# Kernel optimization log

Hardware: AMD Instinct MI355X
Metric: run time of the kernel (lower is better)

Reference implementation:

```python
import jax, jax.numpy as jnp
import numpy as np

N = 16384
K = 16

def _w(k, shape):
    return jax.random.normal(k, shape, jnp.float32) * 0.05

def setup_inputs() -> dict:
    key = jax.random.key(0)
    ks = jax.random.split(key, 20)
    return {
        "img_feat": jax.random.normal(ks[0], (1, 32, N), jnp.float32),
        "cloud": jax.random.uniform(ks[1], (1, N, 3), jnp.float32),
        "conv1_w": _w(ks[2], (64, 32)),   "conv1_b": _w(ks[3], (64,)),
        "conv2_w": _w(ks[4], (128, 64)),  "conv2_b": _w(ks[5], (128,)),
        "psconv1_w": _w(ks[6], (256, 128)), "psconv1_b": _w(ks[7], (256,)),
        "psconv2_w": _w(ks[8], (128, 256)), "psconv2_b": _w(ks[9], (128,)),
        "pconv1_w": _w(ks[10], (64, 3)),  "pconv1_b": _w(ks[11], (64,)),
        "pconv2_w": _w(ks[12], (128, 64)),"pconv2_b": _w(ks[13], (128,)),
        "final_w": _w(ks[14], (32, 416)), "final_b": _w(ks[15], (32,)),
        "topk": K,
    }

def reference(img_feat, cloud, conv1_w, conv1_b, conv2_w, conv2_b,
              psconv1_w, psconv1_b, psconv2_w, psconv2_b,
              pconv1_w, pconv1_b, pconv2_w, pconv2_b,
              final_w, final_b, topk):
    lrelu = lambda x: jax.nn.leaky_relu(x, 0.01)
    pts = cloud[0]            # [N,3]  (module assumes bs=1)
    imf = img_feat[0].T       # [N,32]
    # point MLP: pconv1 -> lrelu -> pconv2 (Conv1d kernel=1 == per-point linear)
    cf = lrelu(pts @ pconv1_w.T + pconv1_b) @ pconv2_w.T + pconv2_b  # [N,128]
    # KNN: k smallest euclidean distances (self included)
    sq = jnp.sum(pts * pts, axis=-1)                 # [N]
    d2 = sq[:, None] + sq[None, :] - 2.0 * (pts @ pts.T)  # [N,N]
    _, idx = jax.lax.top_k(-d2, topk)                # [N,K]
    nb_pts = pts[idx]                                # [N,K,3]
    dist = jnp.sqrt(jnp.maximum(jnp.sum((pts[:, None, :] - nb_pts) ** 2, -1), 1e-12))
    wgt = jax.nn.softmax(-dist, axis=1)              # [N,K]
    nb_img = imf[idx]                                # [N,K,32]
    nb_cf = cf[idx]                                  # [N,K,128]
    sf = lrelu(nb_img @ conv1_w.T + conv1_b) @ conv2_w.T + conv2_b         # [N,K,128]
    sfp = lrelu(nb_cf @ psconv1_w.T + psconv1_b) @ psconv2_w.T + psconv2_b # [N,K,128]
    sf = jnp.max(sf * wgt[:, :, None], axis=1)       # weighted max-pool -> [N,128]
    sfp = jnp.max(sfp * wgt[:, :, None], axis=1)     # [N,128]
    final = jnp.concatenate([sfp, imf, sf, cf], axis=1)  # [N,416]
    out = lrelu(final) @ final_w.T + final_b         # [N,32]
    return out.T[None]                               # [1,32,N]
```

## Files before the change

kernel.cpp:

```cpp
#include <hip/hip_runtime.h>
#include <math.h>

#define N 16384
#define KNN 16
#define G 16
#define NCELL 4096

typedef __attribute__((ext_vector_type(8))) short bf16x8;
typedef __attribute__((ext_vector_type(4))) float f32x4;
typedef unsigned short ushort_t;
typedef unsigned long long u64;

__device__ __forceinline__ float lrelu(float a) { return a > 0.f ? a : 0.01f * a; }

__device__ __forceinline__ ushort_t f2bf(float f) {
  unsigned u = __float_as_uint(f);
  u += 0x7FFF + ((u >> 16) & 1);
  return (ushort_t)(u >> 16);
}
__device__ __forceinline__ float bf2f(ushort_t h) {
  return __uint_as_float((unsigned)h << 16);
}
__device__ __forceinline__ int lanerank(u64 mask) {
  return __builtin_amdgcn_mbcnt_hi((unsigned)(mask >> 32),
         __builtin_amdgcn_mbcnt_lo((unsigned)mask, 0));
}
__device__ __forceinline__ int cellof(float x) {
  int c = (int)(x * (float)G);
  return c < 0 ? 0 : (c > G - 1 ? G - 1 : c);
}

#define PPB 64
__global__ __launch_bounds__(256) void prepw_kernel(
    const float* __restrict__ img, const float* __restrict__ cloud,
    const float* __restrict__ p1w, const float* __restrict__ p1b,
    const float* __restrict__ p2w, const float* __restrict__ p2b,
    const float* __restrict__ ps1w, const float* __restrict__ ps2w,
    const float* __restrict__ c1w, const float* __restrict__ c2w,
    const float* __restrict__ fw,
    float4* __restrict__ pts4, ushort_t* __restrict__ cfh,
    ushort_t* __restrict__ imfh,
    ushort_t* __restrict__ w1h, ushort_t* __restrict__ w2h,
    ushort_t* __restrict__ c1h, ushort_t* __restrict__ c2h,
    float* __restrict__ fwp2, int* __restrict__ count) {
  int t = threadIdx.x;
  if (blockIdx.x >= 256) {
    int e = (blockIdx.x - 256) * 256 + t;
    if (e < 32768) w1h[e] = f2bf(ps1w[e]);
    else if (e < 65536) w2h[e - 32768] = f2bf(ps2w[e - 32768]);
    else if (e < 67584) c1h[e - 65536] = f2bf(c1w[e - 65536]);
    else if (e < 75776) c2h[e - 67584] = f2bf(c2w[e - 67584]);
    else if (e < 89088) {
      int e2 = e - 75776;
      int j4 = e2 >> 7, r2 = e2 & 127;
      int ch = r2 >> 2, sub = r2 & 3;
      fwp2[e2] = fw[ch * 416 + j4 * 4 + sub];
    }
    return;
  }
  __shared__ alignas(16) float w2t[64 * 132];
  __shared__ alignas(16) float hs[PPB * 68];
  __shared__ alignas(16) float w1s[192];
  __shared__ alignas(16) float b1s[64];
  __shared__ alignas(16) float b2s[128];
  __shared__ float ptmp[PPB * 3];
  __shared__ float psx[PPB], psy[PPB], psz[PPB];
  int pb = blockIdx.x * PPB;

  for (int e = t; e < 128 * 64; e += 256) {
    int ch = e >> 6, k = e & 63;
    w2t[k * 132 + ch] = p2w[e];
  }
  if (t < 192) w1s[t] = p1w[t];
  if (t < 64) b1s[t] = p1b[t];
  if (t < 128) b2s[t] = p2b[t];
  if (t < PPB * 3) ptmp[t] = cloud[pb * 3 + t];
  __syncthreads();
  if (t < PPB) {
    float x = ptmp[t * 3], y = ptmp[t * 3 + 1], z = ptmp[t * 3 + 2];
    psx[t] = x; psy[t] = y; psz[t] = z;
    pts4[pb + t] = make_float4(x, y, z, x * x + y * y + z * z);
    int cid = ((cellof(z) << 4) | cellof(y)) << 4 | cellof(x);
    atomicAdd(&count[cid], 1);
  }
  for (int e = t; e < 32 * PPB; e += 256) {
    int c = e >> 6, p = e & 63;
    imfh[(size_t)(pb + p) * 32 + c] = f2bf(img[(size_t)c * N + pb + p]);
  }
  __syncthreads();
  for (int e = t; e < PPB * 64; e += 256) {
    int pt_ = e >> 6, ch = e & 63;
    float a = b1s[ch] + psx[pt_] * w1s[ch * 3] + psy[pt_] * w1s[ch * 3 + 1] +
              psz[pt_] * w1s[ch * 3 + 2];
    hs[pt_ * 68 + ch] = lrelu(a);
  }
  __syncthreads();
  for (int e = t; e < PPB * 32; e += 256) {
    int pt_ = e >> 5, c4 = (e & 31) << 2;
    float4 acc = *(const float4*)&b2s[c4];
    const float* hrow = &hs[pt_ * 68];
    #pragma unroll
    for (int k = 0; k < 64; k += 4) {
      float4 h4 = *(const float4*)&hrow[k];
      float4 w0 = *(const float4*)&w2t[(k + 0) * 132 + c4];
      float4 w1_ = *(const float4*)&w2t[(k + 1) * 132 + c4];
      float4 w2_ = *(const float4*)&w2t[(k + 2) * 132 + c4];
      float4 w3 = *(const float4*)&w2t[(k + 3) * 132 + c4];
      acc.x = fmaf(h4.x, w0.x, fmaf(h4.y, w1_.x, fmaf(h4.z, w2_.x, fmaf(h4.w, w3.x, acc.x))));
      acc.y = fmaf(h4.x, w0.y, fmaf(h4.y, w1_.y, fmaf(h4.z, w2_.y, fmaf(h4.w, w3.y, acc.y))));
      acc.z = fmaf(h4.x, w0.z, fmaf(h4.y, w1_.z, fmaf(h4.z, w2_.z, fmaf(h4.w, w3.z, acc.z))));
      acc.w = fmaf(h4.x, w0.w, fmaf(h4.y, w1_.w, fmaf(h4.z, w2_.w, fmaf(h4.w, w3.w, acc.w))));
    }
    unsigned lo = (unsigned)f2bf(acc.x) | ((unsigned)f2bf(acc.y) << 16);
    unsigned hi = (unsigned)f2bf(acc.z) | ((unsigned)f2bf(acc.w) << 16);
    *(uint2*)&cfh[(size_t)(pb + pt_) * 128 + c4] = make_uint2(lo, hi);
  }
}

__global__ __launch_bounds__(256) void scan_kernel(
    const int* __restrict__ count, int* __restrict__ cellStart,
    int* __restrict__ cellofs) {
  __shared__ int part[256];
  int t = threadIdx.x;
  int local[16];
  int s = 0;
  #pragma unroll
  for (int j = 0; j < 16; ++j) { local[j] = s; s += count[t * 16 + j]; }
  part[t] = s;
  __syncthreads();
  for (int off = 1; off < 256; off <<= 1) {
    int v = (t >= off) ? part[t - off] : 0;
    __syncthreads();
    part[t] += v;
    __syncthreads();
  }
  int base = part[t] - s;
  #pragma unroll
  for (int j = 0; j < 16; ++j) {
    int v = base + local[j];
    cellStart[t * 16 + j] = v;
    cellofs[t * 16 + j] = v;
  }
  if (t == 255) cellStart[NCELL] = part[255];
}

__global__ __launch_bounds__(256) void scatter_kernel(
    const float4* __restrict__ pts4, int* __restrict__ cellofs,
    float4* __restrict__ spts) {
  int p = blockIdx.x * 256 + threadIdx.x;
  float4 v = pts4[p];
  int cid = ((cellof(v.z) << 4) | cellof(v.y)) << 4 | cellof(v.x);
  int pos = atomicAdd(&cellofs[cid], 1);
  spts[pos] = make_float4(v.x, v.y, v.z, __int_as_float(p));
}

#define NB_LD 136
#define S1_LD 264
#define NI_LD 40
#define H1_LD 72
__global__ __launch_bounds__(256) void ymlp_kernel(
    const ushort_t* __restrict__ cfh, const ushort_t* __restrict__ imfh,
    const ushort_t* __restrict__ w1h, const float* __restrict__ b1,
    const ushort_t* __restrict__ w2h, const float* __restrict__ b2,
    const ushort_t* __restrict__ c1h, const float* __restrict__ c1b,
    const ushort_t* __restrict__ c2h, const float* __restrict__ c2b,
    ushort_t* __restrict__ ycf, ushort_t* __restrict__ yimg) {
  __shared__ ushort_t nb[64 * NB_LD];
  __shared__ ushort_t s1[64 * S1_LD];
  int t = threadIdx.x;
  int w = t >> 6, lane = t & 63;
  int col = lane & 15, quad = lane >> 4;

  if (blockIdx.x < 256) {
    int pbase = blockIdx.x * 64;
    for (int e = t; e < 1024; e += 256) {
      int row = e >> 4, c8 = (e & 15) << 3;
      *(uint4*)&nb[row * NB_LD + c8] =
          *(const uint4*)&cfh[(size_t)(pbase + row) * 128 + c8];
    }
    __syncthreads();
    f32x4 acc1[4][4];
    #pragma unroll
    for (int tt = 0; tt < 4; ++tt)
      #pragma unroll
      for (int p = 0; p < 4; ++p) acc1[tt][p] = (f32x4){0.f, 0.f, 0.f, 0.f};
    for (int k0 = 0; k0 < 128; k0 += 32) {
      bf16x8 a[4];
      #pragma unroll
      for (int p = 0; p < 4; ++p)
        a[p] = *(const bf16x8*)&nb[(p * 16 + col) * NB_LD + k0 + quad * 8];
      #pragma unroll
      for (int tt = 0; tt < 4; ++tt) {
        int n = w * 64 + tt * 16 + col;
        bf16x8 b = *(const bf16x8*)&w1h[n * 128 + k0 + quad * 8];
        #pragma unroll
        for (int p = 0; p < 4; ++p)
          acc1[tt][p] = __builtin_amdgcn_mfma_f32_16x16x32_bf16(a[p], b, acc1[tt][p], 0, 0, 0);
      }
    }
    #pragma unroll
    for (int tt = 0; tt < 4; ++tt) {
      int n = w * 64 + tt * 16 + col;
      float bb = b1[n];
      #pragma unroll
      for (int p = 0; p < 4; ++p)
        #pragma unroll
        for (int r = 0; r < 4; ++r)
          s1[(p * 16 + quad * 4 + r) * S1_LD + n] = f2bf(lrelu(acc1[tt][p][r] + bb));
    }
    __syncthreads();
    f32x4 acc2[2][4];
    #pragma unroll
    for (int tt = 0; tt < 2; ++tt)
      #pragma unroll
      for (int p = 0; p < 4; ++p) acc2[tt][p] = (f32x4){0.f, 0.f, 0.f, 0.f};
    for (int k0 = 0; k0 < 256; k0 += 32) {
      bf16x8 a[4];
      #pragma unroll
      for (int p = 0; p < 4; ++p)
        a[p] = *(const bf16x8*)&s1[(p * 16 + col) * S1_LD + k0 + quad * 8];
      #pragma unroll
      for (int tt = 0; tt < 2; ++tt) {
        int n = w * 32 + tt * 16 + col;
        bf16x8 b = *(const bf16x8*)&w2h[n * 256 + k0 + quad * 8];
        #pragma unroll
        for (int p = 0; p < 4; ++p)
          acc2[tt][p] = __builtin_amdgcn_mfma_f32_16x16x32_bf16(a[p], b, acc2[tt][p], 0, 0, 0);
      }
    }
    #pragma unroll
    for (int tt = 0; tt < 2; ++tt) {
      int n = w * 32 + tt * 16 + col;
      float bb = b2[n];
      #pragma unroll
      for (int p = 0; p < 4; ++p)
        #pragma unroll
        for (int r = 0; r < 4; ++r)
          ycf[(size_t)(pbase + p * 16 + quad * 4 + r) * 128 + n] =
              f2bf(acc2[tt][p][r] + bb);
    }
  } else {
    int pbase = (blockIdx.x - 256) * 64;
    ushort_t* nbi = nb;
    ushort_t* h1 = s1;
    {
      int row = t >> 2, c8 = (t & 3) << 3;
      *(uint4*)&nbi[row * NI_LD + c8] =
          *(const uint4*)&imfh[(size_t)(pbase + row) * 32 + c8];
    }
    __syncthreads();
    {
      f32x4 accA[4];
      #pragma unroll
      for (int p = 0; p < 4; ++p) accA[p] = (f32x4){0.f, 0.f, 0.f, 0.f};
      int n = w * 16 + col;
      bf16x8 b = *(const bf16x8*)&c1h[n * 32 + quad * 8];
      #pragma unroll
      for (int p = 0; p < 4; ++p) {
        bf16x8 a = *(const bf16x8*)&nbi[(p * 16 + col) * NI_LD + quad * 8];
        accA[p] = __builtin_amdgcn_mfma_f32_16x16x32_bf16(a, b, accA[p], 0, 0, 0);
      }
      __syncthreads();
      float bb = c1b[n];
      #pragma unroll
      for (int p = 0; p < 4; ++p)
        #pragma unroll
        for (int r = 0; r < 4; ++r)
          h1[(p * 16 + quad * 4 + r) * H1_LD + n] = f2bf(lrelu(accA[p][r] + bb));
    }
    __syncthreads();
    f32x4 acc2[2][4];
    #pragma unroll
    for (int tt = 0; tt < 2; ++tt)
      #pragma unroll
      for (int p = 0; p < 4; ++p) acc2[tt][p] = (f32x4){0.f, 0.f, 0.f, 0.f};
    for (int k0 = 0; k0 < 64; k0 += 32) {
      bf16x8 a[4];
      #pragma unroll
      for (int p = 0; p < 4; ++p)
        a[p] = *(const bf16x8*)&h1[(p * 16 + col) * H1_LD + k0 + quad * 8];
      #pragma unroll
      for (int tt = 0; tt < 2; ++tt) {
        int n = w * 32 + tt * 16 + col;
        bf16x8 b = *(const bf16x8*)&c2h[n * 64 + k0 + quad * 8];
        #pragma unroll
        for (int p = 0; p < 4; ++p)
          acc2[tt][p] = __builtin_amdgcn_mfma_f32_16x16x32_bf16(a[p], b, acc2[tt][p], 0, 0, 0);
      }
    }
    #pragma unroll
    for (int tt = 0; tt < 2; ++tt) {
      int n = w * 32 + tt * 16 + col;
      float bb = c2b[n];
      #pragma unroll
      for (int p = 0; p < 4; ++p)
        #pragma unroll
        for (int r = 0; r < 4; ++r)
          yimg[(size_t)(pbase + p * 16 + quad * 4 + r) * 128 + n] =
              f2bf(acc2[tt][p][r] + bb);
    }
  }
}

__device__ __forceinline__ u64 bsort64(u64 v, int lane) {
  #pragma unroll
  for (int k = 2; k <= 64; k <<= 1) {
    #pragma unroll
    for (int j = k >> 1; j >= 1; j >>= 1) {
      u64 p = __shfl_xor(v, j);
      bool keepmin = (((lane & j) == 0) == ((lane & k) == 0));
      u64 mn = v < p ? v : p;
      u64 mx = v < p ? p : v;
      v = keepmin ? mn : mx;
    }
  }
  return v;
}

__device__ __forceinline__ u64 bclean64(u64 v, int lane) {
  #pragma unroll
  for (int j = 32; j >= 1; j >>= 1) {
    u64 p = __shfl_xor(v, j);
    u64 mn = v < p ? v : p;
    u64 mx = v < p ? p : v;
    v = ((lane & j) == 0) ? mn : mx;
  }
  return v;
}

__device__ __forceinline__ u64 compact_topk(u64* buf, int& cnt, int lane, float& tau) {
  u64 v = (lane < cnt) ? buf[lane] : ~0ULL;
  v = bsort64(v, lane);
  if (cnt > 64) {
    u64 t = (64 + lane < cnt) ? buf[64 + lane] : ~0ULL;
    t = bsort64(t, lane);
    t = __shfl_xor(t, 63);
    v = (t < v) ? t : v;
    v = bclean64(v, lane);
  }
  if (lane < 16) buf[lane] = v;
  cnt = 16;
  u64 k15 = __shfl(v, 15);
  tau = __uint_as_float((unsigned)(k15 >> 32));
  if (!(tau == tau)) tau = INFINITY;
  return v;
}

__device__ __forceinline__ float tadj(float tau, float qw) {
  float a = tau - qw;
  return a + fabsf(a) * 2e-7f + 1e-35f;
}

__global__ __launch_bounds__(256) void knng_kernel(
    const float4* __restrict__ pts4, const float4* __restrict__ spts,
    const int* __restrict__ cellStart,
    const ushort_t* __restrict__ ycf, const ushort_t* __restrict__ yimg,
    const ushort_t* __restrict__ cfh, const ushort_t* __restrict__ imfh,
    const float* __restrict__ fwp2, const float* __restrict__ fb,
    float* __restrict__ out) {
  __shared__ u64 sbuf[4][128];
  __shared__ alignas(16) float feat[4][416];
  int t = threadIdx.x;
  int wv = t >> 6, lane = t & 63;
  int wid = blockIdx.x * 4 + wv;
  u64* buf = sbuf[wv];

  float4 q = pts4[wid];
  float q2x = -2.f * q.x, q2y = -2.f * q.y, q2z = -2.f * q.z, qw = q.w;
  int cx = cellof(q.x), cy = cellof(q.y), cz = cellof(q.z);
  float tau = INFINITY;
  u64 vres;

  for (int r = 1;; ++r) {
    int lx = max(cx - r, 0), hx = min(cx + r, G - 1);
    int ly = max(cy - r, 0), hy = min(cy + r, G - 1);
    int lz = max(cz - r, 0), hz = min(cz + r, G - 1);
    int ny = hy - ly + 1, nz = hz - lz + 1, nruns = ny * nz;
    int cnt = 0;
    float ta = tadj(tau, qw);

    for (int rb = 0; rb < nruns; rb += 64) {
      int ln = rb + lane;
      int rs = 0, rc = 0;
      if (ln < nruns) {
        int z = lz + ln / ny, y = ly + ln % ny;
        int row = ((z << 4) | y) << 4;
        rs = cellStart[row + lx];
        rc = cellStart[row + hx + 1] - rs;
      }
      int off = rc;
      #pragma unroll
      for (int d = 1; d < 64; d <<= 1) {
        int v = __shfl_up(off, d);
        if (lane >= d) off += v;
      }
      int T = __shfl(off, 63);
      off -= rc;

      for (int cb = 0; cb < T; cb += 64) {
        int rk = cb + lane;
        int j = 0;
        #pragma unroll
        for (int step = 32; step; step >>= 1) {
          int nj = j + step;
          int onj = __shfl(off, nj & 63);
          if (nj < 64 && onj <= rk) j = nj;
        }
        int src = __shfl(rs, j) + rk - __shfl(off, j);
        bool valid = rk < T;
        if (!valid) src = 0;
        float4 c = spts[src];
        float cw = fmaf(c.z, c.z, fmaf(c.y, c.y, c.x * c.x));
        float d2 = fmaf(q2x, c.x, fmaf(q2y, c.y, fmaf(q2z, c.z, cw)));
        bool pass = valid && (d2 <= ta);
        u64 mask = __ballot(pass);
        if (mask) {
          if (pass) {
            int oid = __float_as_int(c.w);
            u64 key = ((u64)__float_as_uint(fmaxf(d2 + qw, 0.f)) << 32) | (unsigned)oid;
            buf[cnt + lanerank(mask)] = key;
          }
          cnt += __popcll(mask);
          if (cnt > 64) {
            compact_topk(buf, cnt, lane, tau);
            ta = tadj(tau, qw);
          }
        }
      }
    }
    u64 v = compact_topk(buf, cnt, lane, tau);
    float cl = INFINITY;
    if (lx > 0)     cl = fminf(cl, q.x - (float)lx / (float)G);
    if (hx < G - 1) cl = fminf(cl, (float)(hx + 1) / (float)G - q.x);
    if (ly > 0)     cl = fminf(cl, q.y - (float)ly / (float)G);
    if (hy < G - 1) cl = fminf(cl, (float)(hy + 1) / (float)G - q.y);
    if (lz > 0)     cl = fminf(cl, q.z - (float)lz / (float)G);
    if (hz < G - 1) cl = fminf(cl, (float)(hz + 1) / (float)G - q.z);
    bool full = (lx == 0 && hx == G - 1 && ly == 0 && hy == G - 1 &&
                 lz == 0 && hz == G - 1);
    if (full || tau * 1.00002f <= cl * cl) { vres = v; break; }
  }

  int myid = (lane < KNN) ? (int)(unsigned)(vres & 0xffffffffULL) : 0;
  float mywg = 0.f;
  {
    float4 c = pts4[myid];
    float dx = q.x - c.x, dy = q.y - c.y, dz = q.z - c.z;
    float dist = sqrtf(fmaxf(dx * dx + dy * dy + dz * dz, 1e-12f));
    float md = (lane < KNN) ? dist : INFINITY;
    #pragma unroll
    for (int off = 1; off < KNN; off <<= 1) md = fminf(md, __shfl_xor(md, off));
    float e = expf(md - dist);
    float se = (lane < KNN) ? e : 0.f;
    #pragma unroll
    for (int off = 1; off < KNN; off <<= 1) se += __shfl_xor(se, off);
    mywg = e / se;
  }

  int pid = wid;
  int ksub = lane >> 4, c8 = lane & 15;
  float vimf = (lane < 32) ? bf2f(imfh[(size_t)pid * 32 + lane]) : 0.f;
  unsigned vcf = *(const unsigned*)&cfh[(size_t)pid * 128 + lane * 2];

  float a0[8], a1[8];
  #pragma unroll
  for (int j = 0; j < 8; ++j) { a0[j] = -INFINITY; a1[j] = -INFINITY; }
  #pragma unroll
  for (int kk = 0; kk < 4; ++kk) {
    int k = kk * 4 + ksub;
    int id = __shfl(myid, k);
    float wg = __shfl(mywg, k);
    uint4 v = *(const uint4*)&ycf[(size_t)id * 128 + c8 * 8];
    uint4 u = *(const uint4*)&yimg[(size_t)id * 128 + c8 * 8];
    unsigned vv[4] = {v.x, v.y, v.z, v.w};
    unsigned uu[4] = {u.x, u.y, u.z, u.w};
    #pragma unroll
    for (int h = 0; h < 4; ++h) {
      a0[h * 2]     = fmaxf(a0[h * 2],     bf2f((ushort_t)(vv[h] & 0xffff)) * wg);
      a0[h * 2 + 1] = fmaxf(a0[h * 2 + 1], bf2f((ushort_t)(vv[h] >> 16)) * wg);
      a1[h * 2]     = fmaxf(a1[h * 2],     bf2f((ushort_t)(uu[h] & 0xffff)) * wg);
      a1[h * 2 + 1] = fmaxf(a1[h * 2 + 1], bf2f((ushort_t)(uu[h] >> 16)) * wg);
    }
  }
  #pragma unroll
  for (int j = 0; j < 8; ++j) {
    a0[j] = fmaxf(a0[j], __shfl_xor(a0[j], 16));
    a0[j] = fmaxf(a0[j], __shfl_xor(a0[j], 32));
    a1[j] = fmaxf(a1[j], __shfl_xor(a1[j], 16));
    a1[j] = fmaxf(a1[j], __shfl_xor(a1[j], 32));
  }
  if (lane < 16) {
    #pragma unroll
    for (int j = 0; j < 8; ++j) {
      feat[wv][c8 * 8 + j] = lrelu(a0[j]);
      feat[wv][160 + c8 * 8 + j] = lrelu(a1[j]);
    }
  }
  if (lane < 32) feat[wv][128 + lane] = lrelu(vimf);
  feat[wv][288 + lane * 2] = lrelu(bf2f((ushort_t)(vcf & 0xffff)));
  feat[wv][288 + lane * 2 + 1] = lrelu(bf2f((ushort_t)(vcf >> 16)));

  int ch = lane & 31, half = lane >> 5;
  float acc = half ? 0.f : fb[ch];
  const float* wr = fwp2 + (half * 52) * 128 + ch * 4;
  const float* fr = &feat[wv][half * 208];
  #pragma unroll 4
  for (int j4 = 0; j4 < 52; ++j4) {
    float4 w4 = *(const float4*)(wr + j4 * 128);
    float4 f4 = *(const float4*)(fr + j4 * 4);
    acc = fmaf(f4.x, w4.x, fmaf(f4.y, w4.y, fmaf(f4.z, w4.z, fmaf(f4.w, w4.w, acc))));
  }
  acc += __shfl_xor(acc, 32);
  if (lane < 32) out[(size_t)ch * N + pid] = acc;
}

extern "C" void kernel_launch(void* const* d_in, const int* in_sizes, int n_in,
                              void* d_out, int out_size, void* d_ws, size_t ws_size,
                              hipStream_t stream) {
  const float* img   = (const float*)d_in[0];
  const float* cloud = (const float*)d_in[1];
  const float* c1w   = (const float*)d_in[2];
  const float* c1b   = (const float*)d_in[3];
  const float* c2w   = (const float*)d_in[4];
  const float* c2b   = (const float*)d_in[5];
  const float* ps1w  = (const float*)d_in[6];
  const float* ps1b  = (const float*)d_in[7];
  const float* ps2w  = (const float*)d_in[8];
  const float* ps2b  = (const float*)d_in[9];
  const float* p1w   = (const float*)d_in[10];
  const float* p1b   = (const float*)d_in[11];
  const float* p2w   = (const float*)d_in[12];
  const float* p2b   = (const float*)d_in[13];
  const float* fw    = (const float*)d_in[14];
  const float* fb    = (const float*)d_in[15];
  float* out = (float*)d_out;

  char* ws = (char*)d_ws;
  float4*   pts4  = (float4*)(ws + 0);
  ushort_t* cfh   = (ushort_t*)(ws + 262144);
  ushort_t* imfh  = (ushort_t*)(ws + 4456448);
  ushort_t* w1h   = (ushort_t*)(ws + 7602176);
  ushort_t* w2h   = (ushort_t*)(ws + 7667712);
  ushort_t* c1h   = (ushort_t*)(ws + 7733248);
  ushort_t* c2h   = (ushort_t*)(ws + 7737344);
  ushort_t* ycf   = (ushort_t*)(ws + 7753472);
  ushort_t* yimg  = (ushort_t*)(ws + 11947776);
  float4*   spts  = (float4*)(ws + 16142080);
  int*      cellStart = (int*)(ws + 16404224);
  int*      cellofs   = (int*)(ws + 16436992);
  int*      count     = (int*)(ws + 16453376);
  float*    fwp2      = (float*)(ws + 16469760);

  hipMemsetAsync(count, 0, NCELL * sizeof(int), stream);
  prepw_kernel<<<604, 256, 0, stream>>>(img, cloud, p1w, p1b, p2w, p2b,
                                        ps1w, ps2w, c1w, c2w, fw,
                                        pts4, cfh, imfh, w1h, w2h, c1h, c2h,
                                        fwp2, count);
  scan_kernel<<<1, 256, 0, stream>>>(count, cellStart, cellofs);
  scatter_kernel<<<64, 256, 0, stream>>>(pts4, cellofs, spts);
  ymlp_kernel<<<512, 256, 0, stream>>>(cfh, imfh, w1h, ps1b, w2h, ps2b,
                                       c1h, c1b, c2h, c2b, ycf, yimg);
  knng_kernel<<<N / 4, 256, 0, stream>>>(pts4, spts, cellStart,
                                         ycf, yimg, cfh, imfh,
                                         fwp2, fb, out);
}
```

Baseline: 187.9 us.

## Process KNN queries in spatially sorted order and transpose output separately

The KNN kernel now takes its query points from the cell-sorted array, recovering the original point id from the w field. The sorted order is also swizzled across blocks so that neighbouring waves touch nearby cells and neighbour features, which should improve cache locality and reduce divergence in search radius. Because points arrive out of order, results go to a point-major scratch buffer, and a new transpose kernel writes the channel-major output. The cost is an extra launch plus an extra read and write of the output.

```diff
diff --git a/kernel.cpp b/kernel.cpp
--- a/kernel.cpp
+++ b/kernel.cpp
@@ -357,16 +357,19 @@
     const ushort_t* __restrict__ ycf, const ushort_t* __restrict__ yimg,
     const ushort_t* __restrict__ cfh, const ushort_t* __restrict__ imfh,
     const float* __restrict__ fwp2, const float* __restrict__ fb,
-    float* __restrict__ out) {
+    float* __restrict__ outT) {
   __shared__ u64 sbuf[4][128];
   __shared__ alignas(16) float feat[4][416];
   int t = threadIdx.x;
   int wv = t >> 6, lane = t & 63;
-  int wid = blockIdx.x * 4 + wv;
+  int sblk = (blockIdx.x & 7) * 512 + (blockIdx.x >> 3);
+  int sid = sblk * 4 + wv;
   u64* buf = sbuf[wv];
 
-  float4 q = pts4[wid];
-  float q2x = -2.f * q.x, q2y = -2.f * q.y, q2z = -2.f * q.z, qw = q.w;
+  float4 q = spts[sid];
+  int pid = __float_as_int(q.w);
+  float qw = fmaf(q.z, q.z, fmaf(q.y, q.y, q.x * q.x));
+  float q2x = -2.f * q.x, q2y = -2.f * q.y, q2z = -2.f * q.z;
   int cx = cellof(q.x), cy = cellof(q.y), cz = cellof(q.z);
   float tau = INFINITY;
   u64 vres;
@@ -457,7 +460,6 @@
     mywg = e / se;
   }
 
-  int pid = wid;
   int ksub = lane >> 4, c8 = lane & 15;
   float vimf = (lane < 32) ? bf2f(imfh[(size_t)pid * 32 + lane]) : 0.f;
   unsigned vcf = *(const unsigned*)&cfh[(size_t)pid * 128 + lane * 2];
@@ -511,7 +513,27 @@
     acc = fmaf(f4.x, w4.x, fmaf(f4.y, w4.y, fmaf(f4.z, w4.z, fmaf(f4.w, w4.w, acc))));
   }
   acc += __shfl_xor(acc, 32);
-  if (lane < 32) out[(size_t)ch * N + pid] = acc;
+  if (lane < 32) outT[(size_t)pid * 32 + ch] = acc;
+}
+
+__global__ __launch_bounds__(256) void tran_kernel(
+    const float* __restrict__ outT, float* __restrict__ out) {
+  __shared__ float tile[32][129];
+  int t = threadIdx.x;
+  int pbase = blockIdx.x * 128;
+  #pragma unroll
+  for (int i = 0; i < 16; ++i) {
+    int e = i * 256 + t;
+    int p = e >> 5, c = e & 31;
+    tile[c][p] = outT[(size_t)(pbase + p) * 32 + c];
+  }
+  __syncthreads();
+  #pragma unroll
+  for (int i = 0; i < 16; ++i) {
+    int e = i * 256 + t;
+    int c = e >> 7, p = e & 127;
+    out[(size_t)c * N + pbase + p] = tile[c][p];
+  }
 }
 
 extern "C" void kernel_launch(void* const* d_in, const int* in_sizes, int n_in,
@@ -550,6 +572,7 @@
   int*      cellofs   = (int*)(ws + 16436992);
   int*      count     = (int*)(ws + 16453376);
   float*    fwp2      = (float*)(ws + 16469760);
+  float*    outT      = (float*)(ws + 16523008);
 
   hipMemsetAsync(count, 0, NCELL * sizeof(int), stream);
   prepw_kernel<<<604, 256, 0, stream>>>(img, cloud, p1w, p1b, p2w, p2b,
@@ -562,5 +585,6 @@
                                        c1h, c1b, c2h, c2b, ycf, yimg);
   knng_kernel<<<N / 4, 256, 0, stream>>>(pts4, spts, cellStart,
                                          ycf, yimg, cfh, imfh,
-                                         fwp2, fb, out);
-}
+                                         fwp2, fb, outT);
+  tran_kernel<<<N / 128, 256, 0, stream>>>(outT, out);
+}
```

Measured after the change: 190.1 us. About the same (+1.1%).
